# Performance work log

Hardware: AMD Instinct MI355X
Metric: run time of the kernel (lower is better)

## Reference

```python
import jax, jax.numpy as jnp
import numpy as np

N_HEADS = 16
ROPE_BASE = 10000.0


def _rope(x):
    # x: [B, L, H, Dh]; LLaMA-style rotate-half RoPE, applied over seq dim 1
    B, L, H, Dh = x.shape
    half = Dh // 2
    inv_freq = 1.0 / (ROPE_BASE ** (jnp.arange(0, half, dtype=jnp.float32) / half))
    ang = jnp.arange(L, dtype=jnp.float32)[:, None] * inv_freq[None, :]  # [L, half]
    cos = jnp.concatenate([jnp.cos(ang), jnp.cos(ang)], axis=-1).astype(x.dtype)  # [L, Dh]
    sin = jnp.concatenate([jnp.sin(ang), jnp.sin(ang)], axis=-1).astype(x.dtype)
    cos = cos[None, :, None, :]
    sin = sin[None, :, None, :]
    x1, x2 = x[..., :half], x[..., half:]
    rot = jnp.concatenate([-x2, x1], axis=-1)
    return x * cos + rot * sin


def setup_inputs() -> dict:
    key = jax.random.key(0)
    k1, k2, k3 = jax.random.split(key, 3)
    B, L, D = 2, 2048, 1024
    x = jax.random.normal(k1, (B, L, D), dtype=jnp.float32)
    w_qkv = jax.random.normal(k2, (3 * D, D), dtype=jnp.float32) * (D ** -0.5)
    w_out = jax.random.normal(k3, (D, D), dtype=jnp.float32) * (D ** -0.5)
    return {"x": x, "w_qkv": w_qkv, "w_out": w_out}


def reference(x, w_qkv, w_out):
    B, L, D = x.shape
    H = N_HEADS
    Dh = D // H
    qkv = jnp.einsum('bld,ed->ble', x, w_qkv)  # [B, L, 3D]
    q, k, v = jnp.split(qkv, 3, axis=-1)
    q = q.reshape(B, L, H, Dh)
    k = k.reshape(B, L, H, Dh)
    v = v.reshape(B, L, H, Dh)
    q = _rope(q)
    k = _rope(k)
    scale = 1.0 / jnp.sqrt(jnp.asarray(Dh, dtype=x.dtype))
    scores = jnp.einsum('blhd,bmhd->bhlm', q, k) * scale  # [B, H, L, L]
    attn = jax.nn.softmax(scores, axis=-1)
    out = jnp.einsum('bhlm,bmhd->blhd', attn, v).reshape(B, L, D)
    return jnp.einsum('bld,ed->ble', out, w_out)
```

## Files before the change

kernel.cpp:

```cpp
#include <hip/hip_runtime.h>
#include <hip/hip_bf16.h>
#include <stdint.h>


typedef __attribute__((ext_vector_type(8))) short short8;
typedef __attribute__((ext_vector_type(4))) float floatx4;
typedef __attribute__((ext_vector_type(16))) float floatx16;
typedef __attribute__((ext_vector_type(4))) int intx4;

#define BDIM 2
#define LDIM 2048
#define DDIM 1024
#define HDIM 16
#define DH 64
#define ML (BDIM * LDIM)

#define QSCALE 0.18033688011112042f

__device__ __forceinline__ uint16_t f2b(float x) {
  uint32_t b = __float_as_uint(x);
  b += 0x7FFFu + ((b >> 16) & 1u);
  return (uint16_t)(b >> 16);
}

__device__ __forceinline__ uint32_t pack2(float a, float b) {
  return (uint32_t)f2b(a) | ((uint32_t)f2b(b) << 16);
}

__device__ __forceinline__ uint32_t cvtpk(float lo, float hi) {
  uint32_t r;
  asm("v_cvt_pk_bf16_f32 %0, %1, %2" : "=v"(r) : "v"(lo), "v"(hi));
  return r;
}

#define PLSWAP(a, b) asm("v_permlane32_swap_b32 %0, %1" : "+v"(a), "+v"(b))

__device__ __forceinline__ float max3f(float a, float b, float c) {
  return fmaxf(fmaxf(a, b), c);
}

__device__ __forceinline__ void load_lds_16B(const uint16_t* g, uint16_t* l) {
  __builtin_amdgcn_global_load_lds(
      (const __attribute__((address_space(1))) void*)g,
      (__attribute__((address_space(3))) void*)l, 16, 0, 0);
}

#define WAIT_BAR(N) do {                                         \
    asm volatile("s_waitcnt vmcnt(" #N ")" ::: "memory");        \
    __builtin_amdgcn_sched_barrier(0);                           \
    __builtin_amdgcn_s_barrier();                                \
    asm volatile("" ::: "memory");                               \
    __builtin_amdgcn_sched_barrier(0);                           \
  } while (0)

union I4S8 { intx4 i; short8 s; };

__global__ void prep(const float* __restrict__ x, const float* __restrict__ wqkv,
                     const float* __restrict__ wout,
                     uint16_t* __restrict__ xb, uint16_t* __restrict__ wqkvb,
                     uint16_t* __restrict__ woutb,
                     float* __restrict__ cosT, float* __restrict__ sinT) {
  const int N0 = ML * DDIM / 4;
  const int N1 = 3 * DDIM * DDIM / 4;
  const int N2 = DDIM * DDIM / 4;
  int id = blockIdx.x * 256 + threadIdx.x;
  if (id < N0) {
    float4 v = ((const float4*)x)[id];
    ((uint2*)xb)[id] = make_uint2(pack2(v.x, v.y), pack2(v.z, v.w));
  } else if (id < N0 + N1) {
    int i = id - N0;
    float4 v = ((const float4*)wqkv)[i];
    ((uint2*)wqkvb)[i] = make_uint2(pack2(v.x, v.y), pack2(v.z, v.w));
  } else if (id < N0 + N1 + N2) {
    int i = id - N0 - N1;
    float4 v = ((const float4*)wout)[i];
    ((uint2*)woutb)[i] = make_uint2(pack2(v.x, v.y), pack2(v.z, v.w));
  } else {
    int i = id - N0 - N1 - N2;
    int l = i >> 5, f = i & 31;
    float invf = exp2f(-(float)f * (13.287712379549449f / 32.f));
    float ang = (float)l * invf;
    cosT[i] = cosf(ang);
    sinT[i] = sinf(ang);
  }
}

__device__ __forceinline__ void gemm_step(const uint16_t* __restrict__ as,
                                          const uint16_t* __restrict__ bs,
                                          int wr, int wc, int c0, int c1,
                                          floatx4 (&acc)[4][4]) {
  short8 a[4], b[4];
#pragma unroll
  for (int i = 0; i < 4; ++i)
    a[i] = *(const short8*)&as[(wr * 64 + i * 16 + c0) * 32 + c1 * 8];
#pragma unroll
  for (int j = 0; j < 4; ++j)
    b[j] = *(const short8*)&bs[(wc * 64 + j * 16 + c0) * 32 + c1 * 8];
#pragma unroll
  for (int i = 0; i < 4; ++i)
#pragma unroll
    for (int j = 0; j < 4; ++j)
      acc[i][j] = __builtin_amdgcn_mfma_f32_16x16x32_bf16(a[i], b[j], acc[i][j], 0, 0, 0);
}

#define GEMM_STAGE(BUF, K0) do {                                              \
    const uint16_t* ga = A + (size_t)(m0 + srow) * K + (K0) + scol;           \
    load_lds_16B(ga, &As[(BUF) * 4096 + t * 8]);                              \
    load_lds_16B(ga + (size_t)64 * K, &As[(BUF) * 4096 + 2048 + t * 8]);      \
    const uint16_t* gb = Bm + (size_t)(n0 + srow) * K + (K0) + scol;          \
    load_lds_16B(gb, &Bs[(BUF) * 4096 + t * 8]);                              \
    load_lds_16B(gb + (size_t)64 * K, &Bs[(BUF) * 4096 + 2048 + t * 8]);      \
  } while (0)

__global__ __launch_bounds__(256) void gemm_bt(const uint16_t* __restrict__ A,
                                               const uint16_t* __restrict__ Bm,
                                               float* __restrict__ C,
                                               int M, int N, int K) {
  __shared__ uint16_t As[3 * 4096];
  __shared__ uint16_t Bs[3 * 4096];
  const int m0 = blockIdx.x * 128;
  const int n0 = blockIdx.y * 128;
  const int t = threadIdx.x;
  const int lane = t & 63;
  const int w = t >> 6;
  const int wr = w >> 1, wc = w & 1;
  const int srow = t >> 2;
  const int scol = (t & 3) * 8;
  const int c0 = lane & 15, c1 = lane >> 4;

  floatx4 acc[4][4];
#pragma unroll
  for (int i = 0; i < 4; ++i)
#pragma unroll
    for (int j = 0; j < 4; ++j) acc[i][j] = (floatx4){0.f, 0.f, 0.f, 0.f};

  const int nk = K >> 5;
  GEMM_STAGE(0, 0);
  GEMM_STAGE(1, 32);
#pragma unroll 1
  for (int ki = 0; ki < nk - 1; ++ki) {
    WAIT_BAR(4);
    if (ki + 2 < nk) GEMM_STAGE((ki + 2) % 3, (ki + 2) * 32);
    gemm_step(&As[(ki % 3) * 4096], &Bs[(ki % 3) * 4096], wr, wc, c0, c1, acc);
  }
  WAIT_BAR(0);
  gemm_step(&As[((nk - 1) % 3) * 4096], &Bs[((nk - 1) % 3) * 4096], wr, wc, c0, c1, acc);

#pragma unroll
  for (int i = 0; i < 4; ++i)
#pragma unroll
    for (int j = 0; j < 4; ++j) {
      int row = m0 + wr * 64 + i * 16 + c1 * 4;
      int col = n0 + wc * 64 + j * 16 + c0;
      float* cp = C + (size_t)row * N + col;
#pragma unroll
      for (int r = 0; r < 4; ++r) cp[(size_t)r * N] = acc[i][j][r];
    }
}

__global__ __launch_bounds__(256) void gemm_qkv_rope(const uint16_t* __restrict__ A,
                                                     const uint16_t* __restrict__ Bm,
                                                     const float* __restrict__ cosT,
                                                     const float* __restrict__ sinT,
                                                     uint16_t* __restrict__ qr,
                                                     uint16_t* __restrict__ kr,
                                                     uint16_t* __restrict__ vT) {
  constexpr int K = DDIM;
  __shared__ uint16_t As[3 * 4096];
  __shared__ uint16_t Bs[3 * 4096];
  const int m0 = blockIdx.x * 128;
  const int n0 = blockIdx.y * 128;
  const int t = threadIdx.x;
  const int lane = t & 63;
  const int w = t >> 6;
  const int wr = w >> 1, wc = w & 1;
  const int srow = t >> 2;
  const int scol = (t & 3) * 8;
  const int c0 = lane & 15, c1 = lane >> 4;

  floatx4 acc[4][4];
#pragma unroll
  for (int i = 0; i < 4; ++i)
#pragma unroll
    for (int j = 0; j < 4; ++j) acc[i][j] = (floatx4){0.f, 0.f, 0.f, 0.f};

  const int nk = K >> 5;
  GEMM_STAGE(0, 0);
  GEMM_STAGE(1, 32);
#pragma unroll 1
  for (int ki = 0; ki < nk - 1; ++ki) {
    WAIT_BAR(4);
    if (ki + 2 < nk) GEMM_STAGE((ki + 2) % 3, (ki + 2) * 32);
    gemm_step(&As[(ki % 3) * 4096], &Bs[(ki % 3) * 4096], wr, wc, c0, c1, acc);
  }
  WAIT_BAR(0);
  gemm_step(&As[((nk - 1) % 3) * 4096], &Bs[((nk - 1) % 3) * 4096], wr, wc, c0, c1, acc);

#pragma unroll
  for (int j = 0; j < 4; ++j) {
    const int col = n0 + wc * 64 + j * 16 + c0;
    const int sec = col >> 10;
    const int e = col & 1023;
    const int h = e >> 6, dh = e & 63;
#pragma unroll
    for (int i = 0; i < 4; ++i) {
      const int row = m0 + wr * 64 + i * 16 + c1 * 4;
      const int bb = row >> 11;
      const int l = row & 2047;
      if (sec == 2) {
        uint16_t* vp = vT + ((size_t)((bb * HDIM + h) * DH + dh)) * LDIM + l;
#pragma unroll
        for (int r = 0; r < 4; ++r) vp[r] = f2b(acc[i][j][r]);
      } else {
        const float sgn = (dh < 32) ? -1.f : 1.f;
        const float sc = (sec == 0) ? QSCALE : 1.f;
        uint16_t* dp = (sec == 0 ? qr : kr) + ((size_t)((bb * HDIM + h) * LDIM + l)) * DH + dh;
        const int fi = l * 32 + (dh & 31);
#pragma unroll
        for (int r = 0; r < 4; ++r) {
          float cv = cosT[fi + r * 32];
          float sv = sinT[fi + r * 32];
          float o = (acc[i][j][r] * cv + sgn * acc[i][j ^ 2][r] * sv) * sc;
          dp[(size_t)r * DH] = f2b(o);
        }
      }
    }
  }
}


__device__ __forceinline__ void attn_phase(
    const uint16_t* __restrict__ kt, const uint16_t* __restrict__ vt,
    const int (&off)[2][4], const short8 (&qb)[4],
    float& m, float& lsum, floatx16& acc0, floatx16& acc1) {
  floatx16 s0 = (floatx16){0.f,0.f,0.f,0.f,0.f,0.f,0.f,0.f,0.f,0.f,0.f,0.f,0.f,0.f,0.f,0.f};
  floatx16 s1 = s0;
  __builtin_amdgcn_s_setprio(1);
#pragma unroll
  for (int c = 0; c < 4; ++c) {
    short8 ka = *(const short8*)(kt + off[0][c]);
    s0 = __builtin_amdgcn_mfma_f32_32x32x16_bf16(ka, qb[c], s0, 0, 0, 0);
  }
#pragma unroll
  for (int c = 0; c < 4; ++c) {
    short8 ka = *(const short8*)(kt + off[1][c]);
    s1 = __builtin_amdgcn_mfma_f32_32x32x16_bf16(ka, qb[c], s1, 0, 0, 0);
  }
  __builtin_amdgcn_s_setprio(0);

  float x0 = max3f(s0[0], s0[1], s0[2]);
  float x1 = max3f(s0[3], s0[4], s0[5]);
  float x2 = max3f(s0[6], s0[7], s0[8]);
  float x3 = max3f(s0[9], s0[10], s0[11]);
  float x4 = max3f(s0[12], s0[13], s0[14]);
  float x5 = max3f(s0[15], s1[0], s1[1]);
  float x6 = max3f(s1[2], s1[3], s1[4]);
  float x7 = max3f(s1[5], s1[6], s1[7]);
  float x8 = max3f(s1[8], s1[9], s1[10]);
  float x9 = max3f(s1[11], s1[12], s1[13]);
  float xa = fmaxf(s1[14], s1[15]);
  float y0 = max3f(x0, x1, x2);
  float y1 = max3f(x3, x4, x5);
  float y2 = max3f(x6, x7, x8);
  float y3 = fmaxf(x9, xa);
  float tmax = fmaxf(max3f(y0, y1, y2), y3);
  tmax = fmaxf(tmax, __shfl_xor(tmax, 32));

  if (__any(tmax > m + 8.f)) {
    float mn = fmaxf(m, tmax);
    float scl = __builtin_amdgcn_exp2f(m - mn);
    lsum *= scl;
#pragma unroll
    for (int r = 0; r < 16; ++r) { acc0[r] *= scl; acc1[r] *= scl; }
    m = mn;
  }

  float e[32];
#pragma unroll
  for (int r = 0; r < 16; ++r) e[r] = __builtin_amdgcn_exp2f(s0[r] - m);
#pragma unroll
  for (int r = 0; r < 16; ++r) e[16 + r] = __builtin_amdgcn_exp2f(s1[r] - m);
  float ts0 = 0.f, ts1 = 0.f, ts2 = 0.f, ts3 = 0.f;
#pragma unroll
  for (int r = 0; r < 8; ++r) {
    ts0 += e[r]; ts1 += e[8 + r]; ts2 += e[16 + r]; ts3 += e[24 + r];
  }
  lsum += (ts0 + ts1) + (ts2 + ts3);

  uint32_t w0 = cvtpk(e[0], e[1]),   w1 = cvtpk(e[2], e[3]);
  uint32_t w2 = cvtpk(e[4], e[5]),   w3 = cvtpk(e[6], e[7]);
  uint32_t w4 = cvtpk(e[8], e[9]),   w5 = cvtpk(e[10], e[11]);
  uint32_t w6 = cvtpk(e[12], e[13]), w7 = cvtpk(e[14], e[15]);
  uint32_t w8 = cvtpk(e[16], e[17]), w9 = cvtpk(e[18], e[19]);
  uint32_t wa = cvtpk(e[20], e[21]), wb = cvtpk(e[22], e[23]);
  uint32_t wc_ = cvtpk(e[24], e[25]), wd = cvtpk(e[26], e[27]);
  uint32_t we = cvtpk(e[28], e[29]), wf = cvtpk(e[30], e[31]);
  PLSWAP(w0, w2);  PLSWAP(w1, w3);
  PLSWAP(w4, w6);  PLSWAP(w5, w7);
  PLSWAP(w8, wa);  PLSWAP(w9, wb);
  PLSWAP(wc_, we); PLSWAP(wd, wf);
  I4S8 pf0, pf1, pf2, pf3;
  pf0.i = (intx4){(int)w0, (int)w1, (int)w2, (int)w3};
  pf1.i = (intx4){(int)w4, (int)w5, (int)w6, (int)w7};
  pf2.i = (intx4){(int)w8, (int)w9, (int)wa, (int)wb};
  pf3.i = (intx4){(int)wc_, (int)wd, (int)we, (int)wf};

  __builtin_amdgcn_s_setprio(1);
#pragma unroll
  for (int d = 0; d < 2; ++d) {
    floatx16& ac = d ? acc1 : acc0;
    ac = __builtin_amdgcn_mfma_f32_32x32x16_bf16(*(const short8*)(vt + off[d][0]), pf0.s, ac, 0, 0, 0);
    ac = __builtin_amdgcn_mfma_f32_32x32x16_bf16(*(const short8*)(vt + off[d][1]), pf1.s, ac, 0, 0, 0);
    ac = __builtin_amdgcn_mfma_f32_32x32x16_bf16(*(const short8*)(vt + off[d][2]), pf2.s, ac, 0, 0, 0);
    ac = __builtin_amdgcn_mfma_f32_32x32x16_bf16(*(const short8*)(vt + off[d][3]), pf3.s, ac, 0, 0, 0);
  }
  __builtin_amdgcn_s_setprio(0);
}

__global__ __launch_bounds__(256) void attn(const uint16_t* __restrict__ qr,
                                            const uint16_t* __restrict__ kr,
                                            const uint16_t* __restrict__ vT,
                                            uint16_t* __restrict__ out) {
  __shared__ uint16_t KsA[3 * 4096];
  __shared__ uint16_t VsA[3 * 4096];
  const int t = threadIdx.x, lane = t & 63, w = t >> 6;
  const int l31 = lane & 31, hi = lane >> 5;

  const int id = blockIdx.x;
  const int sw = (id & 7) * 64 + (id >> 3);
  const int bx = sw & 15;
  const int h = (sw >> 4) & 15;
  const int b = sw >> 8;

  const int bh = b * HDIM + h;
  const uint16_t* Qb = qr + (size_t)bh * LDIM * DH;
  const char* Kp = (const char*)(kr + (size_t)bh * LDIM * DH);
  const char* Vp = (const char*)(vT + (size_t)bh * DH * LDIM);

  const int srow = t >> 3;
  const int scsw = ((t & 7) * 16) ^ ((srow & 7) << 4);
  const char* kgs = Kp + (size_t)srow * 128 + scsw;
  const char* vgs = Vp + (size_t)srow * (LDIM * 2) + scsw;

#define STAGE(BUF, N) do {                                                     \
    uint16_t* kd = &KsA[(BUF) * 4096];                                         \
    uint16_t* vd = &VsA[(BUF) * 4096];                                         \
    load_lds_16B((const uint16_t*)(kgs + (size_t)(N) * 8192), &kd[t * 8]);     \
    load_lds_16B((const uint16_t*)(kgs + (size_t)(N) * 8192 + 4096), &kd[2048 + t * 8]); \
    load_lds_16B((const uint16_t*)(vgs + (size_t)(N) * 128), &vd[t * 8]);      \
    load_lds_16B((const uint16_t*)(vgs + (size_t)(N) * 128 + 2 * 32 * LDIM), &vd[2048 + t * 8]); \
  } while (0)

  const int q0 = bx * 128 + w * 32;
  short8 qb[4];
#pragma unroll
  for (int c = 0; c < 4; ++c)
    qb[c] = *(const short8*)&Qb[(size_t)(q0 + l31) * DH + c * 16 + hi * 8];

  const int swz = (l31 & 7) << 4;
  int off[2][4];
#pragma unroll
  for (int x = 0; x < 2; ++x)
#pragma unroll
    for (int c = 0; c < 4; ++c)
      off[x][c] = (x * 32 + l31) * 64 + (((c * 32 + hi * 16) ^ swz) >> 1);

  float m = -1e30f, lsum = 0.f;
  floatx16 acc0 = (floatx16){0.f,0.f,0.f,0.f,0.f,0.f,0.f,0.f,0.f,0.f,0.f,0.f,0.f,0.f,0.f,0.f};
  floatx16 acc1 = acc0;

  STAGE(0, 0);
  STAGE(1, 1);
#pragma unroll 1
  for (int n = 0; n < 31; ++n) {
    WAIT_BAR(4);
    if (n + 2 < 32) STAGE((n + 2) % 3, n + 2);
    attn_phase(&KsA[(n % 3) * 4096], &VsA[(n % 3) * 4096], off, qb,
               m, lsum, acc0, acc1);
  }
  WAIT_BAR(0);
  attn_phase(&KsA[(31 % 3) * 4096], &VsA[(31 % 3) * 4096], off, qb,
             m, lsum, acc0, acc1);
#undef STAGE

  float ltot = lsum + __shfl_xor(lsum, 32);
  float inv = 1.f / ltot;
  size_t orow = (size_t)(b * LDIM) + bx * 128 + w * 32 + l31;
  uint16_t* op = out + orow * DDIM + h * DH;
#pragma unroll
  for (int g = 0; g < 4; ++g) {
    *(uint2*)&op[8 * g + 4 * hi] =
        make_uint2(cvtpk(acc0[4 * g] * inv, acc0[4 * g + 1] * inv),
                   cvtpk(acc0[4 * g + 2] * inv, acc0[4 * g + 3] * inv));
    *(uint2*)&op[32 + 8 * g + 4 * hi] =
        make_uint2(cvtpk(acc1[4 * g] * inv, acc1[4 * g + 1] * inv),
                   cvtpk(acc1[4 * g + 2] * inv, acc1[4 * g + 3] * inv));
  }
}

static constexpr size_t OFF_XB    = 0;
static constexpr size_t OFF_WQKVB = (size_t)8 << 20;
static constexpr size_t OFF_WOUTB = (size_t)14 << 20;
static constexpr size_t OFF_QR    = (size_t)16 << 20;
static constexpr size_t OFF_KR    = (size_t)24 << 20;
static constexpr size_t OFF_VT    = (size_t)32 << 20;
static constexpr size_t OFF_AO    = (size_t)40 << 20;
static constexpr size_t OFF_COS   = (size_t)48 << 20;
static constexpr size_t OFF_SIN   = OFF_COS + ((size_t)256 << 10);

extern "C" void kernel_launch(void* const* d_in, const int* in_sizes, int n_in,
                              void* d_out, int out_size, void* d_ws, size_t ws_size,
                              hipStream_t stream) {
  const float* x     = (const float*)d_in[0];
  const float* w_qkv = (const float*)d_in[1];
  const float* w_out = (const float*)d_in[2];
  float* out = (float*)d_out;
  char* ws = (char*)d_ws;

  uint16_t* xb    = (uint16_t*)(ws + OFF_XB);
  uint16_t* wqkvb = (uint16_t*)(ws + OFF_WQKVB);
  uint16_t* woutb = (uint16_t*)(ws + OFF_WOUTB);
  uint16_t* qr    = (uint16_t*)(ws + OFF_QR);
  uint16_t* kr    = (uint16_t*)(ws + OFF_KR);
  uint16_t* vT    = (uint16_t*)(ws + OFF_VT);
  uint16_t* ao    = (uint16_t*)(ws + OFF_AO);
  float*    cosT  = (float*)(ws + OFF_COS);
  float*    sinT  = (float*)(ws + OFF_SIN);

  prep<<<8448, 256, 0, stream>>>(x, w_qkv, w_out, xb, wqkvb, woutb, cosT, sinT);

  gemm_qkv_rope<<<dim3(ML / 128, 3 * DDIM / 128), 256, 0, stream>>>(xb, wqkvb, cosT, sinT, qr, kr, vT);

  attn<<<512, 256, 0, stream>>>(qr, kr, vT, ao);

  gemm_bt<<<dim3(ML / 128, DDIM / 128), 256, 0, stream>>>(ao, woutb, out, ML, DDIM, DDIM);
}
```

Baseline: 122.9 us.

## Software-pipeline QK of next tile with softmax/PV of current tile

Splits the attention tile step into a QK MFMA phase and a softmax+PV phase, then issues the QK for tile n+1 before the softmax and PV of tile n so that matrix work can overlap the scalar softmax math. LDS staging grows from three to four buffers with a prefetch depth of three, and the loop is unrolled by two to ping-pong the score registers. The cost is more LDS per block and more live registers, which may lower occupancy or cause spills.

```diff
diff --git a/kernel.cpp b/kernel.cpp
--- a/kernel.cpp
+++ b/kernel.cpp
@@ -229,12 +229,12 @@
 }
 
 
-__device__ __forceinline__ void attn_phase(
-    const uint16_t* __restrict__ kt, const uint16_t* __restrict__ vt,
-    const int (&off)[2][4], const short8 (&qb)[4],
-    float& m, float& lsum, floatx16& acc0, floatx16& acc1) {
-  floatx16 s0 = (floatx16){0.f,0.f,0.f,0.f,0.f,0.f,0.f,0.f,0.f,0.f,0.f,0.f,0.f,0.f,0.f,0.f};
-  floatx16 s1 = s0;
+__device__ __forceinline__ void qk_phase(const uint16_t* __restrict__ kt,
+                                         const int (&off)[2][4],
+                                         const short8 (&qb)[4],
+                                         floatx16& s0, floatx16& s1) {
+  floatx16 z = (floatx16){0.f,0.f,0.f,0.f,0.f,0.f,0.f,0.f,0.f,0.f,0.f,0.f,0.f,0.f,0.f,0.f};
+  s0 = z; s1 = z;
   __builtin_amdgcn_s_setprio(1);
 #pragma unroll
   for (int c = 0; c < 4; ++c) {
@@ -247,7 +247,13 @@
     s1 = __builtin_amdgcn_mfma_f32_32x32x16_bf16(ka, qb[c], s1, 0, 0, 0);
   }
   __builtin_amdgcn_s_setprio(0);
-
+}
+
+__device__ __forceinline__ void sm_pv(const uint16_t* __restrict__ vt,
+                                      const int (&off)[2][4],
+                                      floatx16& s0, floatx16& s1,
+                                      float& m, float& lsum,
+                                      floatx16& acc0, floatx16& acc1) {
   float x0 = max3f(s0[0], s0[1], s0[2]);
   float x1 = max3f(s0[3], s0[4], s0[5]);
   float x2 = max3f(s0[6], s0[7], s0[8]);
@@ -321,8 +327,8 @@
                                             const uint16_t* __restrict__ kr,
                                             const uint16_t* __restrict__ vT,
                                             uint16_t* __restrict__ out) {
-  __shared__ uint16_t KsA[3 * 4096];
-  __shared__ uint16_t VsA[3 * 4096];
+  __shared__ uint16_t KsA[4 * 4096];
+  __shared__ uint16_t VsA[4 * 4096];
   const int t = threadIdx.x, lane = t & 63, w = t >> 6;
   const int l31 = lane & 31, hi = lane >> 5;
 
@@ -368,19 +374,27 @@
   float m = -1e30f, lsum = 0.f;
   floatx16 acc0 = (floatx16){0.f,0.f,0.f,0.f,0.f,0.f,0.f,0.f,0.f,0.f,0.f,0.f,0.f,0.f,0.f,0.f};
   floatx16 acc1 = acc0;
-
-  STAGE(0, 0);
-  STAGE(1, 1);
+  floatx16 sA0, sA1, sB0, sB1;
+
+  STAGE(0, 0); STAGE(1, 1); STAGE(2, 2);
+  WAIT_BAR(8);
+  qk_phase(&KsA[0], off, qb, sA0, sA1);
+
+#define BODY(n, CS0, CS1, NS0, NS1, WN) do {                                   \
+    WAIT_BAR(WN);                                                              \
+    if ((n) + 3 < 32) STAGE(((n) + 3) & 3, (n) + 3);                           \
+    qk_phase(&KsA[(((n) + 1) & 3) * 4096], off, qb, NS0, NS1);                 \
+    sm_pv(&VsA[((n) & 3) * 4096], off, CS0, CS1, m, lsum, acc0, acc1);         \
+  } while (0)
+
 #pragma unroll 1
-  for (int n = 0; n < 31; ++n) {
-    WAIT_BAR(4);
-    if (n + 2 < 32) STAGE((n + 2) % 3, n + 2);
-    attn_phase(&KsA[(n % 3) * 4096], &VsA[(n % 3) * 4096], off, qb,
-               m, lsum, acc0, acc1);
-  }
-  WAIT_BAR(0);
-  attn_phase(&KsA[(31 % 3) * 4096], &VsA[(31 % 3) * 4096], off, qb,
-             m, lsum, acc0, acc1);
+  for (int n = 0; n < 30; n += 2) {
+    BODY(n, sA0, sA1, sB0, sB1, 4);
+    BODY(n + 1, sB0, sB1, sA0, sA1, 4);
+  }
+  BODY(30, sA0, sA1, sB0, sB1, 0);
+  sm_pv(&VsA[3 * 4096], off, sB0, sB1, m, lsum, acc0, acc1);
+#undef BODY
 #undef STAGE
 
   float ltot = lsum + __shfl_xor(lsum, 32);
```

After: 121.8 us. No clear change (-0.9%).

## Load K/V tiles directly into registers instead of staging through LDS

Applied to the files above, without the earlier changes.

Drops the shared-memory triple buffer and its barriers. Each wave now loads its own K and V MFMA fragments straight from global memory into registers, double-buffered in registers across iterations. This removes LDS traffic and the per-tile block synchronisation. In exchange, the four waves in a block no longer share loads, so each fetches K/V redundantly from L2/global memory, and register pressure rises. launch_bounds adds a minimum of 2 blocks per CU.

```diff
diff --git a/kernel.cpp b/kernel.cpp
--- a/kernel.cpp
+++ b/kernel.cpp
@@ -229,23 +229,19 @@
 }
 
 
-__device__ __forceinline__ void attn_phase(
-    const uint16_t* __restrict__ kt, const uint16_t* __restrict__ vt,
-    const int (&off)[2][4], const short8 (&qb)[4],
-    float& m, float& lsum, floatx16& acc0, floatx16& acc1) {
+__device__ __forceinline__ void attn_tile(const short8 (&kf)[8], const short8 (&vf)[8],
+                                          const short8 (&qb)[4],
+                                          float& m, float& lsum,
+                                          floatx16& acc0, floatx16& acc1) {
   floatx16 s0 = (floatx16){0.f,0.f,0.f,0.f,0.f,0.f,0.f,0.f,0.f,0.f,0.f,0.f,0.f,0.f,0.f,0.f};
   floatx16 s1 = s0;
   __builtin_amdgcn_s_setprio(1);
 #pragma unroll
-  for (int c = 0; c < 4; ++c) {
-    short8 ka = *(const short8*)(kt + off[0][c]);
-    s0 = __builtin_amdgcn_mfma_f32_32x32x16_bf16(ka, qb[c], s0, 0, 0, 0);
-  }
-#pragma unroll
-  for (int c = 0; c < 4; ++c) {
-    short8 ka = *(const short8*)(kt + off[1][c]);
-    s1 = __builtin_amdgcn_mfma_f32_32x32x16_bf16(ka, qb[c], s1, 0, 0, 0);
-  }
+  for (int c = 0; c < 4; ++c)
+    s0 = __builtin_amdgcn_mfma_f32_32x32x16_bf16(kf[c], qb[c], s0, 0, 0, 0);
+#pragma unroll
+  for (int c = 0; c < 4; ++c)
+    s1 = __builtin_amdgcn_mfma_f32_32x32x16_bf16(kf[4 + c], qb[c], s1, 0, 0, 0);
   __builtin_amdgcn_s_setprio(0);
 
   float x0 = max3f(s0[0], s0[1], s0[2]);
@@ -306,23 +302,21 @@
   pf3.i = (intx4){(int)wc_, (int)wd, (int)we, (int)wf};
 
   __builtin_amdgcn_s_setprio(1);
-#pragma unroll
-  for (int d = 0; d < 2; ++d) {
-    floatx16& ac = d ? acc1 : acc0;
-    ac = __builtin_amdgcn_mfma_f32_32x32x16_bf16(*(const short8*)(vt + off[d][0]), pf0.s, ac, 0, 0, 0);
-    ac = __builtin_amdgcn_mfma_f32_32x32x16_bf16(*(const short8*)(vt + off[d][1]), pf1.s, ac, 0, 0, 0);
-    ac = __builtin_amdgcn_mfma_f32_32x32x16_bf16(*(const short8*)(vt + off[d][2]), pf2.s, ac, 0, 0, 0);
-    ac = __builtin_amdgcn_mfma_f32_32x32x16_bf16(*(const short8*)(vt + off[d][3]), pf3.s, ac, 0, 0, 0);
-  }
+  acc0 = __builtin_amdgcn_mfma_f32_32x32x16_bf16(vf[0], pf0.s, acc0, 0, 0, 0);
+  acc0 = __builtin_amdgcn_mfma_f32_32x32x16_bf16(vf[1], pf1.s, acc0, 0, 0, 0);
+  acc0 = __builtin_amdgcn_mfma_f32_32x32x16_bf16(vf[2], pf2.s, acc0, 0, 0, 0);
+  acc0 = __builtin_amdgcn_mfma_f32_32x32x16_bf16(vf[3], pf3.s, acc0, 0, 0, 0);
+  acc1 = __builtin_amdgcn_mfma_f32_32x32x16_bf16(vf[4], pf0.s, acc1, 0, 0, 0);
+  acc1 = __builtin_amdgcn_mfma_f32_32x32x16_bf16(vf[5], pf1.s, acc1, 0, 0, 0);
+  acc1 = __builtin_amdgcn_mfma_f32_32x32x16_bf16(vf[6], pf2.s, acc1, 0, 0, 0);
+  acc1 = __builtin_amdgcn_mfma_f32_32x32x16_bf16(vf[7], pf3.s, acc1, 0, 0, 0);
   __builtin_amdgcn_s_setprio(0);
 }
 
-__global__ __launch_bounds__(256) void attn(const uint16_t* __restrict__ qr,
-                                            const uint16_t* __restrict__ kr,
-                                            const uint16_t* __restrict__ vT,
-                                            uint16_t* __restrict__ out) {
-  __shared__ uint16_t KsA[3 * 4096];
-  __shared__ uint16_t VsA[3 * 4096];
+__global__ __launch_bounds__(256, 2) void attn(const uint16_t* __restrict__ qr,
+                                               const uint16_t* __restrict__ kr,
+                                               const uint16_t* __restrict__ vT,
+                                               uint16_t* __restrict__ out) {
   const int t = threadIdx.x, lane = t & 63, w = t >> 6;
   const int l31 = lane & 31, hi = lane >> 5;
 
@@ -337,18 +331,18 @@
   const char* Kp = (const char*)(kr + (size_t)bh * LDIM * DH);
   const char* Vp = (const char*)(vT + (size_t)bh * DH * LDIM);
 
-  const int srow = t >> 3;
-  const int scsw = ((t & 7) * 16) ^ ((srow & 7) << 4);
-  const char* kgs = Kp + (size_t)srow * 128 + scsw;
-  const char* vgs = Vp + (size_t)srow * (LDIM * 2) + scsw;
-
-#define STAGE(BUF, N) do {                                                     \
-    uint16_t* kd = &KsA[(BUF) * 4096];                                         \
-    uint16_t* vd = &VsA[(BUF) * 4096];                                         \
-    load_lds_16B((const uint16_t*)(kgs + (size_t)(N) * 8192), &kd[t * 8]);     \
-    load_lds_16B((const uint16_t*)(kgs + (size_t)(N) * 8192 + 4096), &kd[2048 + t * 8]); \
-    load_lds_16B((const uint16_t*)(vgs + (size_t)(N) * 128), &vd[t * 8]);      \
-    load_lds_16B((const uint16_t*)(vgs + (size_t)(N) * 128 + 2 * 32 * LDIM), &vd[2048 + t * 8]); \
+  const char* kb = Kp + (size_t)l31 * 128 + hi * 16;
+  const char* vb = Vp + (size_t)l31 * 4096 + hi * 16;
+
+#define LOADT(KF, VF, N) do {                                                  \
+    size_t ko = (size_t)(N) * 8192, vo = (size_t)(N) * 128;                    \
+    _Pragma("unroll")                                                          \
+    for (int c = 0; c < 4; ++c) {                                              \
+      KF[c]     = *(const short8*)(kb + ko + c * 32);                          \
+      KF[4 + c] = *(const short8*)(kb + ko + 4096 + c * 32);                   \
+      VF[c]     = *(const short8*)(vb + vo + c * 32);                          \
+      VF[4 + c] = *(const short8*)(vb + vo + 131072 + c * 32);                 \
+    }                                                                          \
   } while (0)
 
   const int q0 = bx * 128 + w * 32;
@@ -356,32 +350,24 @@
 #pragma unroll
   for (int c = 0; c < 4; ++c)
     qb[c] = *(const short8*)&Qb[(size_t)(q0 + l31) * DH + c * 16 + hi * 8];
-
-  const int swz = (l31 & 7) << 4;
-  int off[2][4];
-#pragma unroll
-  for (int x = 0; x < 2; ++x)
-#pragma unroll
-    for (int c = 0; c < 4; ++c)
-      off[x][c] = (x * 32 + l31) * 64 + (((c * 32 + hi * 16) ^ swz) >> 1);
 
   float m = -1e30f, lsum = 0.f;
   floatx16 acc0 = (floatx16){0.f,0.f,0.f,0.f,0.f,0.f,0.f,0.f,0.f,0.f,0.f,0.f,0.f,0.f,0.f,0.f};
   floatx16 acc1 = acc0;
-
-  STAGE(0, 0);
-  STAGE(1, 1);
+  short8 kA[8], vA[8], kB[8], vB[8];
+
+  LOADT(kA, vA, 0);
 #pragma unroll 1
-  for (int n = 0; n < 31; ++n) {
-    WAIT_BAR(4);
-    if (n + 2 < 32) STAGE((n + 2) % 3, n + 2);
-    attn_phase(&KsA[(n % 3) * 4096], &VsA[(n % 3) * 4096], off, qb,
-               m, lsum, acc0, acc1);
-  }
-  WAIT_BAR(0);
-  attn_phase(&KsA[(31 % 3) * 4096], &VsA[(31 % 3) * 4096], off, qb,
-             m, lsum, acc0, acc1);
-#undef STAGE
+  for (int n = 0; n < 30; n += 2) {
+    LOADT(kB, vB, n + 1);
+    attn_tile(kA, vA, qb, m, lsum, acc0, acc1);
+    LOADT(kA, vA, n + 2);
+    attn_tile(kB, vB, qb, m, lsum, acc0, acc1);
+  }
+  LOADT(kB, vB, 31);
+  attn_tile(kA, vA, qb, m, lsum, acc0, acc1);
+  attn_tile(kB, vB, qb, m, lsum, acc0, acc1);
+#undef LOADT
 
   float ltot = lsum + __shfl_xor(lsum, 32);
   float inv = 1.f / ltot;
```

Result: slower. 186.5 us (+51.8%).
